# Kernel tuning notes

Hardware: AMD Instinct MI355X
Metric: run time of the kernel (lower is better)

The kernel has to match this reference:

```python
import jax, jax.numpy as jnp
import numpy as np

K = 16          # number of nearest neighbors (init kwarg k)
EPS = 1e-3      # denom threshold from the original code


def setup_inputs() -> dict:
    key = jax.random.key(0)
    k1, k2, k3 = jax.random.split(key, 3)
    V, F = 5000, 10000
    vertices = jax.random.normal(k1, (V, 3), dtype=jnp.float32)
    faces = jax.random.randint(k2, (F, 3), 0, V)
    probabilities = jax.random.uniform(k3, (F,), dtype=jnp.float32)
    return {"vertices": vertices, "faces": faces, "probabilities": probabilities}


def reference(vertices, faces, probabilities):
    F = faces.shape[0]
    pos = vertices[faces]                       # [F,3,3] triangle vertex coords
    bary = pos.mean(axis=1)                     # [F,3] barycenters

    # brute-force kNN over barycenters (x == y, so self is included like torch_geometric knn)
    sq = jnp.sum(bary * bary, axis=-1)          # [F]
    d2 = sq[:, None] + sq[None, :] - 2.0 * (bary @ bary.T)   # [F,F]
    _, nbr = jax.lax.top_k(-d2, K)              # [F,K] neighbor face indices

    # face normals
    e1 = pos[:, 1] - pos[:, 0]
    e2 = pos[:, 2] - pos[:, 0]
    n = jnp.cross(e1, e2)
    n = n / jnp.maximum(jnp.linalg.norm(n, axis=-1, keepdims=True), 1e-12)  # [F,3]

    # per (tri, neighbor, triangle-edge) plane intersection test
    nb_pos = pos[nbr]                           # [F,K,3,3] neighbor triangle vertices
    l0 = nb_pos                                 # segment starts
    l1 = jnp.roll(nb_pos, -1, axis=2)           # segment ends (k -> (k+1)%3)
    n_b = n[:, None, None, :]                   # [F,1,1,3]
    p0_b = pos[:, 0][:, None, None, :]          # [F,1,1,3] plane point of tri

    denom = jnp.sum(n_b * (l1 - l0), axis=-1)   # [F,K,3]
    numer = jnp.sum(n_b * (p0_b - l0), axis=-1) # [F,K,3]
    safe_denom = jnp.where(jnp.abs(denom) < EPS, 1.0, denom)
    t = numer / safe_denom
    hit = (jnp.abs(denom) >= EPS) & (t > 0.0) & (t < 1.0)   # [F,K,3]

    # early break in original => at most 1 increment per (tri, neighbor) pair
    pen = jnp.any(hit, axis=-1) & (nbr != jnp.arange(F)[:, None])  # [F,K]

    # scatter-add penetrations into neighbor_idx
    faces_penetrated = jnp.zeros((F,), jnp.float32).at[nbr.ravel()].add(
        pen.ravel().astype(jnp.float32))

    return jnp.dot(probabilities, faces_penetrated) / F
```

## Files before the change

### kernel.cpp

```cpp
#include <hip/hip_runtime.h>
#include <math.h>

#define KNN 16
#define EPS_F 0.001f
#define BLK 256
#define SCH 8
#define SSTRIDE 4

#define REP16(M) M(0) M(1) M(2) M(3) M(4) M(5) M(6) M(7) \
                 M(8) M(9) M(10) M(11) M(12) M(13) M(14) M(15)

#define CEAI(p,a,b) { int _lo = min(p##a, p##b); int _hi = max(p##a, p##b); p##a = _lo; p##b = _hi; }
#define CEDI(p,a,b) { int _lo = min(p##a, p##b); int _hi = max(p##a, p##b); p##a = _hi; p##b = _lo; }

#define SORT16I(p) \
  CEAI(p,0,1) CEDI(p,2,3) CEAI(p,4,5) CEDI(p,6,7) CEAI(p,8,9) CEDI(p,10,11) CEAI(p,12,13) CEDI(p,14,15) \
  CEAI(p,0,2) CEAI(p,1,3) CEDI(p,4,6) CEDI(p,5,7) CEAI(p,8,10) CEAI(p,9,11) CEDI(p,12,14) CEDI(p,13,15) \
  CEAI(p,0,1) CEAI(p,2,3) CEDI(p,4,5) CEDI(p,6,7) CEAI(p,8,9) CEAI(p,10,11) CEDI(p,12,13) CEDI(p,14,15) \
  CEAI(p,0,4) CEAI(p,1,5) CEAI(p,2,6) CEAI(p,3,7) CEDI(p,8,12) CEDI(p,9,13) CEDI(p,10,14) CEDI(p,11,15) \
  CEAI(p,0,2) CEAI(p,1,3) CEAI(p,4,6) CEAI(p,5,7) CEDI(p,8,10) CEDI(p,9,11) CEDI(p,12,14) CEDI(p,13,15) \
  CEAI(p,0,1) CEAI(p,2,3) CEAI(p,4,5) CEAI(p,6,7) CEDI(p,8,9) CEDI(p,10,11) CEDI(p,12,13) CEDI(p,14,15) \
  CEAI(p,0,8) CEAI(p,1,9) CEAI(p,2,10) CEAI(p,3,11) CEAI(p,4,12) CEAI(p,5,13) CEAI(p,6,14) CEAI(p,7,15) \
  CEAI(p,0,4) CEAI(p,1,5) CEAI(p,2,6) CEAI(p,3,7) CEAI(p,8,12) CEAI(p,9,13) CEAI(p,10,14) CEAI(p,11,15) \
  CEAI(p,0,2) CEAI(p,1,3) CEAI(p,4,6) CEAI(p,5,7) CEAI(p,8,10) CEAI(p,9,11) CEAI(p,12,14) CEAI(p,13,15) \
  CEAI(p,0,1) CEAI(p,2,3) CEAI(p,4,5) CEAI(p,6,7) CEAI(p,8,9) CEAI(p,10,11) CEAI(p,12,13) CEAI(p,14,15)

#define RESORT16I(p) \
  CEAI(p,0,8) CEAI(p,1,9) CEAI(p,2,10) CEAI(p,3,11) CEAI(p,4,12) CEAI(p,5,13) CEAI(p,6,14) CEAI(p,7,15) \
  CEAI(p,0,4) CEAI(p,1,5) CEAI(p,2,6) CEAI(p,3,7) CEAI(p,8,12) CEAI(p,9,13) CEAI(p,10,14) CEAI(p,11,15) \
  CEAI(p,0,2) CEAI(p,1,3) CEAI(p,4,6) CEAI(p,5,7) CEAI(p,8,10) CEAI(p,9,11) CEAI(p,12,14) CEAI(p,13,15) \
  CEAI(p,0,1) CEAI(p,2,3) CEAI(p,4,5) CEAI(p,6,7) CEAI(p,8,9) CEAI(p,10,11) CEAI(p,12,13) CEAI(p,14,15)

#define MERGE16I(r,x) \
  r##0=min(r##0,x##15); r##1=min(r##1,x##14); r##2=min(r##2,x##13); r##3=min(r##3,x##12); \
  r##4=min(r##4,x##11); r##5=min(r##5,x##10); r##6=min(r##6,x##9);  r##7=min(r##7,x##8);  \
  r##8=min(r##8,x##7);  r##9=min(r##9,x##6);  r##10=min(r##10,x##5); r##11=min(r##11,x##4); \
  r##12=min(r##12,x##3); r##13=min(r##13,x##2); r##14=min(r##14,x##1); r##15=min(r##15,x##0); \
  RESORT16I(r)

__device__ __forceinline__ float distf(float4 q, float4 P) {
    return fmaf(q.x, P.x, fmaf(q.y, P.y, fmaf(q.z, P.z, q.w + P.w)));
}
__device__ __forceinline__ int packkey(float d2, int j) {
    return (__float_as_int(d2) & 0xFFFFC000) | j;
}

__global__ __launch_bounds__(BLK) void prep_kernel(
    const float* __restrict__ verts, const int* __restrict__ faces,
    float4* __restrict__ baryq, float4* __restrict__ baryqm,
    float* __restrict__ nrm, float* __restrict__ p0s, int F)
{
    int f = blockIdx.x * BLK + threadIdx.x;
    if (f >= F) return;
    int i0 = faces[3*f+0], i1 = faces[3*f+1], i2 = faces[3*f+2];
    float ax = verts[3*i0+0], ay = verts[3*i0+1], az = verts[3*i0+2];
    float bx = verts[3*i1+0], by = verts[3*i1+1], bz = verts[3*i1+2];
    float cx = verts[3*i2+0], cy = verts[3*i2+1], cz = verts[3*i2+2];
    float gx = (ax + bx + cx) / 3.0f;
    float gy = (ay + by + cy) / 3.0f;
    float gz = (az + bz + cz) / 3.0f;
    float sq = gx*gx + gy*gy + gz*gz;
    baryq[f]  = make_float4(gx, gy, gz, sq);
    baryqm[f] = make_float4(-2.0f*gx, -2.0f*gy, -2.0f*gz, sq);
    float e1x = bx-ax, e1y = by-ay, e1z = bz-az;
    float e2x = cx-ax, e2y = cy-ay, e2z = cz-az;
    float nx = e1y*e2z - e1z*e2y;
    float ny = e1z*e2x - e1x*e2z;
    float nz = e1x*e2y - e1y*e2x;
    float len = sqrtf(nx*nx + ny*ny + nz*nz);
    float dn = fmaxf(len, 1e-12f);
    nrm[3*f+0] = nx/dn; nrm[3*f+1] = ny/dn; nrm[3*f+2] = nz/dn;
    p0s[3*f+0] = ax; p0s[3*f+1] = ay; p0s[3*f+2] = az;
}

__global__ __launch_bounds__(BLK) void knn_sample(
    const float4* __restrict__ baryq, const float4* __restrict__ baryqm,
    int* __restrict__ samp_k, int F, int SLEN)
{
    extern __shared__ float4 sb[];
    int tid = threadIdx.x;
    int qi = blockIdx.x * BLK + tid;
    float4 q = baryq[min(qi, F-1)];
    #define DECLR(m) int r##m = 0x7fffffff;
    REP16(DECLR)
    #undef DECLR
    int sbase = blockIdx.y * SLEN;
    for (int s = tid; s < SLEN; s += BLK) {
        int j = (sbase + s) * SSTRIDE;
        sb[s] = (j < F) ? baryqm[j] : make_float4(0.f, 0.f, 0.f, INFINITY);
    }
    __syncthreads();
    #pragma unroll 1
    for (int g = 0; g < SLEN; g += 16) {
        #define MKK(m) int x##m = packkey(distf(q, sb[g+(m)]), (sbase+g+(m))*SSTRIDE);
        REP16(MKK)
        #undef MKK
        SORT16I(x)
        MERGE16I(r, x)
    }
    if (qi < F) {
        size_t cb = (size_t)blockIdx.y * KNN * F + qi;
        #define STR(m) samp_k[cb + (size_t)(m) * F] = r##m;
        REP16(STR)
        #undef STR
    }
}

__global__ __launch_bounds__(BLK) void merge_T(
    const int* __restrict__ samp_k, int* __restrict__ Tkey,
    int* __restrict__ cnt, float* __restrict__ out, int F)
{
    int qi = blockIdx.x * BLK + threadIdx.x;
    if (blockIdx.x == 0 && threadIdx.x == 0) out[0] = 0.0f;
    if (qi >= F) return;
    #define LDR(m) int r##m = samp_k[(size_t)(m) * F + qi];
    REP16(LDR)
    #undef LDR
    #pragma unroll 2
    for (int c = 1; c < SCH; ++c) {
        size_t cb = (size_t)c * KNN * F + qi;
        #define LDX(m) int x##m = samp_k[cb + (size_t)(m) * F];
        REP16(LDX)
        #undef LDX
        MERGE16I(r, x)
    }
    Tkey[qi] = r15;
    cnt[qi] = 0;
}

__global__ __launch_bounds__(BLK, 8) void collect_kernel(
    const float4* __restrict__ baryq, const float4* __restrict__ baryqm,
    const int* __restrict__ Tkey, int* __restrict__ cnt,
    int* __restrict__ buf, int F, int CLEN, int CAP)
{
    int tid = threadIdx.x;
    int qi = blockIdx.x * BLK + tid;
    bool active = qi < F;
    int qc = min(qi, F-1);
    float4 q = baryq[qc];
    int T = active ? Tkey[qc] : 0x80000000;
    int Tup = T | 0x3FFF;
    int s0=0,s1=0,s2=0,s3=0,s4=0,s5=0,s6=0,s7=0;
    int lcnt = 0;
    #define SHIFT_INS(keyv) { \
        s7=s6; s6=s5; s5=s4; s4=s3; s3=s2; s2=s1; s1=s0; s0=(keyv); \
        if (++lcnt == 8 && active) { \
            int bp = atomicAdd(&cnt[qi], 8); \
            if (bp + 8 <= CAP) { \
                buf[(size_t)(bp+0)*F+qi]=s0; buf[(size_t)(bp+1)*F+qi]=s1; \
                buf[(size_t)(bp+2)*F+qi]=s2; buf[(size_t)(bp+3)*F+qi]=s3; \
                buf[(size_t)(bp+4)*F+qi]=s4; buf[(size_t)(bp+5)*F+qi]=s5; \
                buf[(size_t)(bp+6)*F+qi]=s6; buf[(size_t)(bp+7)*F+qi]=s7; } \
            lcnt = 0; } }
    int jb = blockIdx.y * CLEN;
    int je = min(jb + CLEN, F);
    int jfull = jb + ((je - jb) & ~15);
    #pragma unroll 1
    for (int base = jb; base < jfull; base += 16) {
        const float4* tp = baryqm + base;
        #define CSTEP(m) { float4 P = tp[m]; \
            float d = distf(q, P); \
            if (__float_as_int(d) <= Tup) { \
                int key = packkey(d, base + (m)); \
                SHIFT_INS(key) } }
        REP16(CSTEP)
        #undef CSTEP
    }
    for (int j = jfull; j < je; ++j) {
        float4 P = baryqm[j];
        float d = distf(q, P);
        if (__float_as_int(d) <= Tup) {
            int key = packkey(d, j);
            SHIFT_INS(key)
        }
    }
    #undef SHIFT_INS
    if (active && lcnt > 0) {
        int bp = atomicAdd(&cnt[qi], lcnt);
        #define FLUSH(m) if ((m) < lcnt && bp + (m) < CAP) \
            buf[(size_t)(bp + (m)) * F + qi] = s##m;
        FLUSH(0) FLUSH(1) FLUSH(2) FLUSH(3) FLUSH(4) FLUSH(5) FLUSH(6) FLUSH(7)
        #undef FLUSH
    }
}

__device__ __forceinline__ bool edge_test(
    float nx, float ny, float nz, float px, float py, float pz,
    float ax, float ay, float az, float bx, float by, float bz)
{
    float denom = nx*(bx-ax) + ny*(by-ay) + nz*(bz-az);
    if (fabsf(denom) < EPS_F) return false;
    float numer = nx*(px-ax) + ny*(py-ay) + nz*(pz-az);
    float t = numer / denom;
    return (t > 0.0f) && (t < 1.0f);
}

__global__ __launch_bounds__(BLK) void select_pen(
    const int* __restrict__ buf, const int* __restrict__ cnt,
    const float* __restrict__ verts, const int* __restrict__ faces,
    const float* __restrict__ prob, const float* __restrict__ nrm,
    const float* __restrict__ p0s, float* __restrict__ out,
    int F, int CAP)
{
    int qi = blockIdx.x * BLK + threadIdx.x;
    float val = 0.0f;
    if (qi < F) {
        int n = min(cnt[qi], CAP);
        #define DECLR(m) int r##m = 0x7fffffff;
        REP16(DECLR)
        #undef DECLR
        #pragma unroll 1
        for (int t = 0; t < n; t += 16) {
            #define LSEL(m) int x##m; { int v = buf[(size_t)(t + (m)) * F + qi]; \
                x##m = (t + (m) < n) ? v : 0x7fffffff; }
            REP16(LSEL)
            #undef LSEL
            SORT16I(x)
            MERGE16I(r, x)
        }
        float nx = nrm[3*qi+0], ny = nrm[3*qi+1], nz = nrm[3*qi+2];
        float px = p0s[3*qi+0], py = p0s[3*qi+1], pz = p0s[3*qi+2];
        #define PENM(m) { int j = r##m & 0x3FFF; \
            if (j != qi && j < F) { \
                int j0 = faces[3*j+0], j1 = faces[3*j+1], j2 = faces[3*j+2]; \
                float ax = verts[3*j0+0], ay = verts[3*j0+1], az = verts[3*j0+2]; \
                float bx = verts[3*j1+0], by = verts[3*j1+1], bz = verts[3*j1+2]; \
                float cx = verts[3*j2+0], cy = verts[3*j2+1], cz = verts[3*j2+2]; \
                bool hit = edge_test(nx,ny,nz, px,py,pz, ax,ay,az, bx,by,bz) \
                        || edge_test(nx,ny,nz, px,py,pz, bx,by,bz, cx,cy,cz) \
                        || edge_test(nx,ny,nz, px,py,pz, cx,cy,cz, ax,ay,az); \
                if (hit) val += prob[j]; } }
        REP16(PENM)
        #undef PENM
    }
    __shared__ float red[BLK];
    red[threadIdx.x] = val;
    __syncthreads();
    #pragma unroll
    for (int s = BLK/2; s > 0; s >>= 1) {
        if (threadIdx.x < s) red[threadIdx.x] += red[threadIdx.x + s];
        __syncthreads();
    }
    if (threadIdx.x == 0) atomicAdd(out, red[0] / (float)F);
}

extern "C" void kernel_launch(void* const* d_in, const int* in_sizes, int n_in,
                              void* d_out, int out_size, void* d_ws, size_t ws_size,
                              hipStream_t stream)
{
    const float* verts = (const float*)d_in[0];
    const int*   faces = (const int*)d_in[1];
    const float* prob  = (const float*)d_in[2];
    float* out = (float*)d_out;
    int F = in_sizes[2];

    size_t off = 0;
    auto carve = [&](size_t bytes) {
        size_t cur = off;
        off += (bytes + 255) & ~(size_t)255;
        return cur;
    };
    char* w = (char*)d_ws;
    int qBlocks = (F + BLK - 1) / BLK;
    float4* baryq  = (float4*)(w + carve((size_t)F * sizeof(float4)));
    float4* baryqm = (float4*)(w + carve((size_t)F * sizeof(float4)));
    float*  nrm    = (float*)(w + carve((size_t)F * 3 * sizeof(float)));
    float*  p0s    = (float*)(w + carve((size_t)F * 3 * sizeof(float)));
    int*    Tkey   = (int*)(w + carve((size_t)F * sizeof(int)));
    int*    cnt    = (int*)(w + carve((size_t)F * sizeof(int)));
    int*    samp_k = (int*)(w + carve((size_t)SCH * KNN * F * sizeof(int)));

    size_t remain = (ws_size > off) ? (ws_size - off) : 0;
    int CAP = (int)(remain / ((size_t)F * sizeof(int))) - 16;
    if (CAP > 448) CAP = 448;
    if (CAP < 256) CAP = 256;
    CAP &= ~15;
    int* buf = (int*)(w + carve((size_t)F * (CAP + 16) * sizeof(int)));

    int nSamp = (F + SSTRIDE - 1) / SSTRIDE;
    int SLEN = ((nSamp + SCH - 1) / SCH + 15) & ~15;
    int nChTarget = (2048 / qBlocks > 1) ? (2048 / qBlocks) : 1;
    int CLEN = (((F + nChTarget - 1) / nChTarget) + 15) & ~15;
    int nCChunk = (F + CLEN - 1) / CLEN;

    prep_kernel<<<qBlocks, BLK, 0, stream>>>(verts, faces, baryq, baryqm, nrm, p0s, F);
    knn_sample<<<dim3(qBlocks, SCH), BLK, SLEN * sizeof(float4), stream>>>(
        baryq, baryqm, samp_k, F, SLEN);
    merge_T<<<qBlocks, BLK, 0, stream>>>(samp_k, Tkey, cnt, out, F);
    collect_kernel<<<dim3(qBlocks, nCChunk), BLK, 0, stream>>>(
        baryq, baryqm, Tkey, cnt, buf, F, CLEN, CAP);
    select_pen<<<qBlocks, BLK, 0, stream>>>(
        buf, cnt, verts, faces, prob, nrm, p0s, out, F, CAP);
}
```

Measured before the change: 86.73 us.

## Sort barycenters by z-bins and restrict kNN candidate scan to z-window

Builds a histogram of barycenters by z coordinate, scans it, and scatters points into z-sorted order. Each query block then derives a distance threshold from 256 nearby sorted samples and computes a z window from the block's maximum radius. Candidate collection scans only that window instead of all F points. This removes most of the O(F^2) distance work and the separate sample-merge pass, at the cost of several extra small kernels, atomics in the histogram and scatter, and sensitivity to how points are spread along z.

```diff
diff --git a/kernel.cpp b/kernel.cpp
--- a/kernel.cpp
+++ b/kernel.cpp
@@ -4,8 +4,10 @@
 #define KNN 16
 #define EPS_F 0.001f
 #define BLK 256
-#define SCH 8
-#define SSTRIDE 4
+#define NBIN 2048
+#define ZMIN -8.0f
+#define ZMAX 8.0f
+#define NC 24
 
 #define REP16(M) M(0) M(1) M(2) M(3) M(4) M(5) M(6) M(7) \
                  M(8) M(9) M(10) M(11) M(12) M(13) M(14) M(15)
@@ -44,11 +46,16 @@
 __device__ __forceinline__ int packkey(float d2, int j) {
     return (__float_as_int(d2) & 0xFFFFC000) | j;
 }
+__device__ __forceinline__ int binOf(float z) {
+    int b = (int)((z - ZMIN) * ((float)NBIN / (ZMAX - ZMIN)));
+    return min(max(b, 0), NBIN - 1);
+}
 
 __global__ __launch_bounds__(BLK) void prep_kernel(
     const float* __restrict__ verts, const int* __restrict__ faces,
     float4* __restrict__ baryq, float4* __restrict__ baryqm,
-    float* __restrict__ nrm, float* __restrict__ p0s, int F)
+    float* __restrict__ nrm, float* __restrict__ p0s,
+    int* __restrict__ hist, int F)
 {
     int f = blockIdx.x * BLK + threadIdx.x;
     if (f >= F) return;
@@ -62,6 +69,7 @@
     float sq = gx*gx + gy*gy + gz*gz;
     baryq[f]  = make_float4(gx, gy, gz, sq);
     baryqm[f] = make_float4(-2.0f*gx, -2.0f*gy, -2.0f*gz, sq);
+    atomicAdd(&hist[binOf(gz)], 1);
     float e1x = bx-ax, e1y = by-ay, e1z = bz-az;
     float e2x = cx-ax, e2y = cy-ay, e2z = cz-az;
     float nx = e1y*e2z - e1z*e2y;
@@ -73,113 +81,167 @@
     p0s[3*f+0] = ax; p0s[3*f+1] = ay; p0s[3*f+2] = az;
 }
 
-__global__ __launch_bounds__(BLK) void knn_sample(
+__global__ __launch_bounds__(BLK) void scan_kernel(
+    const int* __restrict__ hist, int* __restrict__ binStart,
+    int* __restrict__ binCur, int F)
+{
+    __shared__ int part[BLK];
+    int tid = threadIdx.x;
+    int base = tid * (NBIN / BLK);
+    int s = 0;
+    #pragma unroll
+    for (int i = 0; i < NBIN / BLK; ++i) s += hist[base + i];
+    part[tid] = s;
+    __syncthreads();
+    for (int off = 1; off < BLK; off <<= 1) {
+        int v = (tid >= off) ? part[tid - off] : 0;
+        __syncthreads();
+        part[tid] += v;
+        __syncthreads();
+    }
+    int run = part[tid] - s;
+    #pragma unroll
+    for (int i = 0; i < NBIN / BLK; ++i) {
+        binStart[base + i] = run;
+        binCur[base + i] = run;
+        run += hist[base + i];
+    }
+    if (tid == BLK - 1) binStart[NBIN] = run;
+}
+
+__global__ __launch_bounds__(BLK) void scatter_kernel(
     const float4* __restrict__ baryq, const float4* __restrict__ baryqm,
-    int* __restrict__ samp_k, int F, int SLEN)
-{
-    extern __shared__ float4 sb[];
+    int* __restrict__ binCur, float4* __restrict__ sq,
+    float4* __restrict__ sqm, int* __restrict__ sor, int F)
+{
+    int f = blockIdx.x * BLK + threadIdx.x;
+    if (f >= F) return;
+    float4 bq = baryq[f];
+    int pos = atomicAdd(&binCur[binOf(bq.z)], 1);
+    sq[pos] = bq;
+    sqm[pos] = baryqm[f];
+    sor[pos] = f;
+}
+
+__global__ __launch_bounds__(BLK) void sampleT_kernel(
+    const float4* __restrict__ sq, const float4* __restrict__ sqm,
+    const int* __restrict__ sor, const int* __restrict__ binStart,
+    int* __restrict__ Tkey, int* __restrict__ cnt,
+    int* __restrict__ blockLoHi, float* __restrict__ out, int F)
+{
+    __shared__ float4 sb[256];
+    __shared__ int sio[256];
+    __shared__ float redf[BLK];
     int tid = threadIdx.x;
-    int qi = blockIdx.x * BLK + tid;
-    float4 q = baryq[min(qi, F-1)];
+    int B = blockIdx.x * BLK;
+    int p = B + tid;
+    bool active = p < F;
+    int pc = min(p, F - 1);
+    float4 q = sq[pc];
+    int SN = min(256, F);
+    int sp = min(F, 1024);
+    int stride = max(1, sp / SN);
+    int ws = B + BLK/2 - (SN * stride) / 2;
+    ws = max(0, min(ws, F - SN * stride));
+    for (int s = tid; s < SN; s += BLK) {
+        int j = ws + s * stride;
+        sb[s] = sqm[j];
+        sio[s] = sor[j];
+    }
+    for (int s = SN + tid; s < 256; s += BLK) {
+        sb[s] = make_float4(0.f, 0.f, 0.f, INFINITY);
+        sio[s] = 0x3FFF;
+    }
+    __syncthreads();
     #define DECLR(m) int r##m = 0x7fffffff;
     REP16(DECLR)
     #undef DECLR
-    int sbase = blockIdx.y * SLEN;
-    for (int s = tid; s < SLEN; s += BLK) {
-        int j = (sbase + s) * SSTRIDE;
-        sb[s] = (j < F) ? baryqm[j] : make_float4(0.f, 0.f, 0.f, INFINITY);
-    }
-    __syncthreads();
     #pragma unroll 1
-    for (int g = 0; g < SLEN; g += 16) {
-        #define MKK(m) int x##m = packkey(distf(q, sb[g+(m)]), (sbase+g+(m))*SSTRIDE);
+    for (int g = 0; g < 256; g += 16) {
+        #define MKK(m) int x##m = packkey(distf(q, sb[g+(m)]), sio[g+(m)]);
         REP16(MKK)
         #undef MKK
         SORT16I(x)
         MERGE16I(r, x)
     }
-    if (qi < F) {
-        size_t cb = (size_t)blockIdx.y * KNN * F + qi;
-        #define STR(m) samp_k[cb + (size_t)(m) * F] = r##m;
-        REP16(STR)
-        #undef STR
-    }
-}
-
-__global__ __launch_bounds__(BLK) void merge_T(
-    const int* __restrict__ samp_k, int* __restrict__ Tkey,
-    int* __restrict__ cnt, float* __restrict__ out, int F)
-{
-    int qi = blockIdx.x * BLK + threadIdx.x;
-    if (blockIdx.x == 0 && threadIdx.x == 0) out[0] = 0.0f;
-    if (qi >= F) return;
-    #define LDR(m) int r##m = samp_k[(size_t)(m) * F + qi];
-    REP16(LDR)
-    #undef LDR
-    #pragma unroll 2
-    for (int c = 1; c < SCH; ++c) {
-        size_t cb = (size_t)c * KNN * F + qi;
-        #define LDX(m) int x##m = samp_k[cb + (size_t)(m) * F];
-        REP16(LDX)
-        #undef LDX
-        MERGE16I(r, x)
-    }
-    Tkey[qi] = r15;
-    cnt[qi] = 0;
+    int T = r15;
+    if (active) { Tkey[p] = T; cnt[p] = 0; }
+    float zr = active ? (sqrtf(fmaxf(__int_as_float(T | 0x3FFF), 0.f)) + 1e-3f) : 0.f;
+    redf[tid] = zr;
+    __syncthreads();
+    #pragma unroll
+    for (int s = BLK/2; s > 0; s >>= 1) {
+        if (tid < s) redf[tid] = fmaxf(redf[tid], redf[tid + s]);
+        __syncthreads();
+    }
+    if (tid == 0) {
+        float rmax = redf[0];
+        float zlo = sq[B].z - rmax;
+        float zhi = sq[min(B + BLK, F) - 1].z + rmax;
+        int lo = binStart[binOf(zlo)];
+        int hi = binStart[binOf(zhi) + 1];
+        blockLoHi[2*blockIdx.x]   = lo;
+        blockLoHi[2*blockIdx.x+1] = hi;
+        if (blockIdx.x == 0) out[0] = 0.f;
+    }
 }
 
 __global__ __launch_bounds__(BLK, 8) void collect_kernel(
-    const float4* __restrict__ baryq, const float4* __restrict__ baryqm,
-    const int* __restrict__ Tkey, int* __restrict__ cnt,
-    int* __restrict__ buf, int F, int CLEN, int CAP)
+    const float4* __restrict__ sq, const float4* __restrict__ sqm,
+    const int* __restrict__ sor, const int* __restrict__ Tkey,
+    const int* __restrict__ blockLoHi, int* __restrict__ cnt,
+    int* __restrict__ buf, int F, int CAP)
 {
     int tid = threadIdx.x;
-    int qi = blockIdx.x * BLK + tid;
-    bool active = qi < F;
-    int qc = min(qi, F-1);
-    float4 q = baryq[qc];
-    int T = active ? Tkey[qc] : 0x80000000;
+    int B = blockIdx.x * BLK;
+    int p = B + tid;
+    bool active = p < F;
+    int pc = min(p, F - 1);
+    float4 q = sq[pc];
+    int T = active ? Tkey[pc] : 0x80000000;
     int Tup = T | 0x3FFF;
-    int s0=0,s1=0,s2=0,s3=0,s4=0,s5=0,s6=0,s7=0;
+    int lo = blockLoHi[2*blockIdx.x], hi = blockLoHi[2*blockIdx.x+1];
+    int step = (((hi - lo + NC - 1) / NC) + 15) & ~15;
+    int jb = lo + blockIdx.y * step;
+    if (jb >= hi) return;
+    int je = min(jb + step, hi);
+    int s0 = 0, s1 = 0, s2 = 0, s3 = 0;
     int lcnt = 0;
     #define SHIFT_INS(keyv) { \
-        s7=s6; s6=s5; s5=s4; s4=s3; s3=s2; s2=s1; s1=s0; s0=(keyv); \
-        if (++lcnt == 8 && active) { \
-            int bp = atomicAdd(&cnt[qi], 8); \
-            if (bp + 8 <= CAP) { \
-                buf[(size_t)(bp+0)*F+qi]=s0; buf[(size_t)(bp+1)*F+qi]=s1; \
-                buf[(size_t)(bp+2)*F+qi]=s2; buf[(size_t)(bp+3)*F+qi]=s3; \
-                buf[(size_t)(bp+4)*F+qi]=s4; buf[(size_t)(bp+5)*F+qi]=s5; \
-                buf[(size_t)(bp+6)*F+qi]=s6; buf[(size_t)(bp+7)*F+qi]=s7; } \
+        s3 = s2; s2 = s1; s1 = s0; s0 = (keyv); \
+        if (++lcnt == 4 && active) { \
+            int bp = atomicAdd(&cnt[p], 4); \
+            if (bp + 4 <= CAP) { \
+                buf[(size_t)(bp+0)*F+p] = s0; buf[(size_t)(bp+1)*F+p] = s1; \
+                buf[(size_t)(bp+2)*F+p] = s2; buf[(size_t)(bp+3)*F+p] = s3; } \
             lcnt = 0; } }
-    int jb = blockIdx.y * CLEN;
-    int je = min(jb + CLEN, F);
     int jfull = jb + ((je - jb) & ~15);
     #pragma unroll 1
     for (int base = jb; base < jfull; base += 16) {
-        const float4* tp = baryqm + base;
+        const float4* tp = sqm + base;
+        const int* to = sor + base;
         #define CSTEP(m) { float4 P = tp[m]; \
             float d = distf(q, P); \
             if (__float_as_int(d) <= Tup) { \
-                int key = packkey(d, base + (m)); \
+                int key = packkey(d, to[m]); \
                 SHIFT_INS(key) } }
         REP16(CSTEP)
         #undef CSTEP
     }
     for (int j = jfull; j < je; ++j) {
-        float4 P = baryqm[j];
+        float4 P = sqm[j];
         float d = distf(q, P);
         if (__float_as_int(d) <= Tup) {
-            int key = packkey(d, j);
+            int key = packkey(d, sor[j]);
             SHIFT_INS(key)
         }
     }
     #undef SHIFT_INS
     if (active && lcnt > 0) {
-        int bp = atomicAdd(&cnt[qi], lcnt);
+        int bp = atomicAdd(&cnt[p], lcnt);
         #define FLUSH(m) if ((m) < lcnt && bp + (m) < CAP) \
-            buf[(size_t)(bp + (m)) * F + qi] = s##m;
-        FLUSH(0) FLUSH(1) FLUSH(2) FLUSH(3) FLUSH(4) FLUSH(5) FLUSH(6) FLUSH(7)
+            buf[(size_t)(bp + (m)) * F + p] = s##m;
+        FLUSH(0) FLUSH(1) FLUSH(2) FLUSH(3)
         #undef FLUSH
     }
 }
@@ -197,31 +259,33 @@
 
 __global__ __launch_bounds__(BLK) void select_pen(
     const int* __restrict__ buf, const int* __restrict__ cnt,
+    const int* __restrict__ sor,
     const float* __restrict__ verts, const int* __restrict__ faces,
     const float* __restrict__ prob, const float* __restrict__ nrm,
     const float* __restrict__ p0s, float* __restrict__ out,
     int F, int CAP)
 {
-    int qi = blockIdx.x * BLK + threadIdx.x;
+    int p = blockIdx.x * BLK + threadIdx.x;
     float val = 0.0f;
-    if (qi < F) {
-        int n = min(cnt[qi], CAP);
+    if (p < F) {
+        int oq = sor[p];
+        int n = min(cnt[p], CAP);
         #define DECLR(m) int r##m = 0x7fffffff;
         REP16(DECLR)
         #undef DECLR
         #pragma unroll 1
         for (int t = 0; t < n; t += 16) {
-            #define LSEL(m) int x##m; { int v = buf[(size_t)(t + (m)) * F + qi]; \
+            #define LSEL(m) int x##m; { int v = buf[(size_t)(t + (m)) * F + p]; \
                 x##m = (t + (m) < n) ? v : 0x7fffffff; }
             REP16(LSEL)
             #undef LSEL
             SORT16I(x)
             MERGE16I(r, x)
         }
-        float nx = nrm[3*qi+0], ny = nrm[3*qi+1], nz = nrm[3*qi+2];
-        float px = p0s[3*qi+0], py = p0s[3*qi+1], pz = p0s[3*qi+2];
+        float nx = nrm[3*oq+0], ny = nrm[3*oq+1], nz = nrm[3*oq+2];
+        float px = p0s[3*oq+0], py = p0s[3*oq+1], pz = p0s[3*oq+2];
         #define PENM(m) { int j = r##m & 0x3FFF; \
-            if (j != qi && j < F) { \
+            if (j != oq && j < F) { \
                 int j0 = faces[3*j+0], j1 = faces[3*j+1], j2 = faces[3*j+2]; \
                 float ax = verts[3*j0+0], ay = verts[3*j0+1], az = verts[3*j0+2]; \
                 float bx = verts[3*j1+0], by = verts[3*j1+1], bz = verts[3*j1+2]; \
@@ -262,13 +326,19 @@
     };
     char* w = (char*)d_ws;
     int qBlocks = (F + BLK - 1) / BLK;
-    float4* baryq  = (float4*)(w + carve((size_t)F * sizeof(float4)));
-    float4* baryqm = (float4*)(w + carve((size_t)F * sizeof(float4)));
-    float*  nrm    = (float*)(w + carve((size_t)F * 3 * sizeof(float)));
-    float*  p0s    = (float*)(w + carve((size_t)F * 3 * sizeof(float)));
-    int*    Tkey   = (int*)(w + carve((size_t)F * sizeof(int)));
-    int*    cnt    = (int*)(w + carve((size_t)F * sizeof(int)));
-    int*    samp_k = (int*)(w + carve((size_t)SCH * KNN * F * sizeof(int)));
+    float4* baryq   = (float4*)(w + carve((size_t)F * sizeof(float4)));
+    float4* baryqm  = (float4*)(w + carve((size_t)F * sizeof(float4)));
+    float*  nrm     = (float*)(w + carve((size_t)F * 3 * sizeof(float)));
+    float*  p0s     = (float*)(w + carve((size_t)F * 3 * sizeof(float)));
+    int*    hist    = (int*)(w + carve((size_t)NBIN * sizeof(int)));
+    int*    binStart= (int*)(w + carve((size_t)(NBIN + 1) * sizeof(int)));
+    int*    binCur  = (int*)(w + carve((size_t)NBIN * sizeof(int)));
+    float4* sq      = (float4*)(w + carve((size_t)F * sizeof(float4)));
+    float4* sqm     = (float4*)(w + carve((size_t)F * sizeof(float4)));
+    int*    sor     = (int*)(w + carve((size_t)F * sizeof(int)));
+    int*    Tkey    = (int*)(w + carve((size_t)F * sizeof(int)));
+    int*    cnt     = (int*)(w + carve((size_t)F * sizeof(int)));
+    int*    blockLoHi = (int*)(w + carve((size_t)2 * qBlocks * sizeof(int)));
 
     size_t remain = (ws_size > off) ? (ws_size - off) : 0;
     int CAP = (int)(remain / ((size_t)F * sizeof(int))) - 16;
@@ -277,18 +347,16 @@
     CAP &= ~15;
     int* buf = (int*)(w + carve((size_t)F * (CAP + 16) * sizeof(int)));
 
-    int nSamp = (F + SSTRIDE - 1) / SSTRIDE;
-    int SLEN = ((nSamp + SCH - 1) / SCH + 15) & ~15;
-    int nChTarget = (2048 / qBlocks > 1) ? (2048 / qBlocks) : 1;
-    int CLEN = (((F + nChTarget - 1) / nChTarget) + 15) & ~15;
-    int nCChunk = (F + CLEN - 1) / CLEN;
-
-    prep_kernel<<<qBlocks, BLK, 0, stream>>>(verts, faces, baryq, baryqm, nrm, p0s, F);
-    knn_sample<<<dim3(qBlocks, SCH), BLK, SLEN * sizeof(float4), stream>>>(
-        baryq, baryqm, samp_k, F, SLEN);
-    merge_T<<<qBlocks, BLK, 0, stream>>>(samp_k, Tkey, cnt, out, F);
-    collect_kernel<<<dim3(qBlocks, nCChunk), BLK, 0, stream>>>(
-        baryq, baryqm, Tkey, cnt, buf, F, CLEN, CAP);
+    hipMemsetAsync(hist, 0, NBIN * sizeof(int), stream);
+    prep_kernel<<<qBlocks, BLK, 0, stream>>>(
+        verts, faces, baryq, baryqm, nrm, p0s, hist, F);
+    scan_kernel<<<1, BLK, 0, stream>>>(hist, binStart, binCur, F);
+    scatter_kernel<<<qBlocks, BLK, 0, stream>>>(
+        baryq, baryqm, binCur, sq, sqm, sor, F);
+    sampleT_kernel<<<qBlocks, BLK, 0, stream>>>(
+        sq, sqm, sor, binStart, Tkey, cnt, blockLoHi, out, F);
+    collect_kernel<<<dim3(qBlocks, NC), BLK, 0, stream>>>(
+        sq, sqm, sor, Tkey, blockLoHi, cnt, buf, F, CAP);
     select_pen<<<qBlocks, BLK, 0, stream>>>(
-        buf, cnt, verts, faces, prob, nrm, p0s, out, F, CAP);
-}
+        buf, cnt, sor, verts, faces, prob, nrm, p0s, out, F, CAP);
+}
```

New measurement: 235.3 us. 171% more time.

## Fuse threshold merge into collect kernel and add wave-uniform insert branch

Applied to the files above, without the earlier changes.

Removes the separate merge_T kernel: each collect block now recomputes the per-query k-th distance threshold from the sampled candidate lists, and cnt/out zeroing moves into the prep kernel. This saves one kernel launch and the Tkey round trip through global memory. In exchange, the merge (128 loads and sorting-network merges per query) is repeated in every column-chunk block. The candidate insert is also guarded by a wavefront-wide __any test so waves can skip the branch uniformly.

```diff
diff --git a/kernel.cpp b/kernel.cpp
--- a/kernel.cpp
+++ b/kernel.cpp
@@ -48,10 +48,13 @@
 __global__ __launch_bounds__(BLK) void prep_kernel(
     const float* __restrict__ verts, const int* __restrict__ faces,
     float4* __restrict__ baryq, float4* __restrict__ baryqm,
-    float* __restrict__ nrm, float* __restrict__ p0s, int F)
+    float* __restrict__ nrm, float* __restrict__ p0s,
+    int* __restrict__ cnt, float* __restrict__ out, int F)
 {
     int f = blockIdx.x * BLK + threadIdx.x;
     if (f >= F) return;
+    if (f == 0) out[0] = 0.0f;
+    cnt[f] = 0;
     int i0 = faces[3*f+0], i1 = faces[3*f+1], i2 = faces[3*f+2];
     float ax = verts[3*i0+0], ay = verts[3*i0+1], az = verts[3*i0+2];
     float bx = verts[3*i1+0], by = verts[3*i1+1], bz = verts[3*i1+2];
@@ -106,31 +109,9 @@
     }
 }
 
-__global__ __launch_bounds__(BLK) void merge_T(
-    const int* __restrict__ samp_k, int* __restrict__ Tkey,
-    int* __restrict__ cnt, float* __restrict__ out, int F)
-{
-    int qi = blockIdx.x * BLK + threadIdx.x;
-    if (blockIdx.x == 0 && threadIdx.x == 0) out[0] = 0.0f;
-    if (qi >= F) return;
-    #define LDR(m) int r##m = samp_k[(size_t)(m) * F + qi];
-    REP16(LDR)
-    #undef LDR
-    #pragma unroll 2
-    for (int c = 1; c < SCH; ++c) {
-        size_t cb = (size_t)c * KNN * F + qi;
-        #define LDX(m) int x##m = samp_k[cb + (size_t)(m) * F];
-        REP16(LDX)
-        #undef LDX
-        MERGE16I(r, x)
-    }
-    Tkey[qi] = r15;
-    cnt[qi] = 0;
-}
-
 __global__ __launch_bounds__(BLK, 8) void collect_kernel(
     const float4* __restrict__ baryq, const float4* __restrict__ baryqm,
-    const int* __restrict__ Tkey, int* __restrict__ cnt,
+    const int* __restrict__ samp_k, int* __restrict__ cnt,
     int* __restrict__ buf, int F, int CLEN, int CAP)
 {
     int tid = threadIdx.x;
@@ -138,8 +119,22 @@
     bool active = qi < F;
     int qc = min(qi, F-1);
     float4 q = baryq[qc];
-    int T = active ? Tkey[qc] : 0x80000000;
-    int Tup = T | 0x3FFF;
+    int T;
+    {
+        #define LDR(m) int r##m = samp_k[(size_t)(m) * F + qc];
+        REP16(LDR)
+        #undef LDR
+        #pragma unroll 2
+        for (int c = 1; c < SCH; ++c) {
+            size_t cb = (size_t)c * KNN * F + qc;
+            #define LDX(m) int x##m = samp_k[cb + (size_t)(m) * F];
+            REP16(LDX)
+            #undef LDX
+            MERGE16I(r, x)
+        }
+        T = r15;
+    }
+    int Tup = active ? (T | 0x3FFF) : 0x80000000;
     int s0=0,s1=0,s2=0,s3=0,s4=0,s5=0,s6=0,s7=0;
     int lcnt = 0;
     #define SHIFT_INS(keyv) { \
@@ -160,18 +155,18 @@
         const float4* tp = baryqm + base;
         #define CSTEP(m) { float4 P = tp[m]; \
             float d = distf(q, P); \
-            if (__float_as_int(d) <= Tup) { \
-                int key = packkey(d, base + (m)); \
-                SHIFT_INS(key) } }
+            bool h = __float_as_int(d) <= Tup; \
+            if (__any(h)) { \
+                if (h) { int key = packkey(d, base + (m)); SHIFT_INS(key) } } }
         REP16(CSTEP)
         #undef CSTEP
     }
     for (int j = jfull; j < je; ++j) {
         float4 P = baryqm[j];
         float d = distf(q, P);
-        if (__float_as_int(d) <= Tup) {
-            int key = packkey(d, j);
-            SHIFT_INS(key)
+        bool h = __float_as_int(d) <= Tup;
+        if (__any(h)) {
+            if (h) { int key = packkey(d, j); SHIFT_INS(key) }
         }
     }
     #undef SHIFT_INS
@@ -266,7 +261,6 @@
     float4* baryqm = (float4*)(w + carve((size_t)F * sizeof(float4)));
     float*  nrm    = (float*)(w + carve((size_t)F * 3 * sizeof(float)));
     float*  p0s    = (float*)(w + carve((size_t)F * 3 * sizeof(float)));
-    int*    Tkey   = (int*)(w + carve((size_t)F * sizeof(int)));
     int*    cnt    = (int*)(w + carve((size_t)F * sizeof(int)));
     int*    samp_k = (int*)(w + carve((size_t)SCH * KNN * F * sizeof(int)));
 
@@ -283,12 +277,12 @@
     int CLEN = (((F + nChTarget - 1) / nChTarget) + 15) & ~15;
     int nCChunk = (F + CLEN - 1) / CLEN;
 
-    prep_kernel<<<qBlocks, BLK, 0, stream>>>(verts, faces, baryq, baryqm, nrm, p0s, F);
+    prep_kernel<<<qBlocks, BLK, 0, stream>>>(
+        verts, faces, baryq, baryqm, nrm, p0s, cnt, out, F);
     knn_sample<<<dim3(qBlocks, SCH), BLK, SLEN * sizeof(float4), stream>>>(
         baryq, baryqm, samp_k, F, SLEN);
-    merge_T<<<qBlocks, BLK, 0, stream>>>(samp_k, Tkey, cnt, out, F);
     collect_kernel<<<dim3(qBlocks, nCChunk), BLK, 0, stream>>>(
-        baryq, baryqm, Tkey, cnt, buf, F, CLEN, CAP);
+        baryq, baryqm, samp_k, cnt, buf, F, CLEN, CAP);
     select_pen<<<qBlocks, BLK, 0, stream>>>(
         buf, cnt, verts, faces, prob, nrm, p0s, out, F, CAP);
 }
```

Result: slower. 96.88 us (+11.7%).
